# Kernel tuning notes

Measured on AMD Instinct MI355X. Metric: run time of the kernel, lower is better.

## Reference

```python
import jax, jax.numpy as jnp
import numpy as np
import math

B, S, D, H = 256, 200, 256, 8
DH = D // H
EPS = 1e-6
GELU_C = math.sqrt(2.0 / math.pi)


def layer_norm(x, a, b):
    # torch LayerNorm variant: unbiased std, eps added to std (not var)
    mean = jnp.mean(x, axis=-1, keepdims=True)
    std = jnp.sqrt(jnp.var(x, axis=-1, keepdims=True, ddof=1))
    return a * (x - mean) / (std + EPS) + b


def setup_inputs() -> dict:
    key = jax.random.key(0)
    ks = jax.random.split(key, 12)
    s = 0.02
    return {
        "hidden_img": jax.random.normal(ks[0], (B, S, D), jnp.float32),
        "hidden_title": jax.random.normal(ks[1], (B, S, D), jnp.float32),
        "mask": jax.random.randint(ks[2], (B, S), 0, 2, jnp.int32),
        "a_img": jnp.ones((D,), jnp.float32),
        "b_img": jnp.zeros((D,), jnp.float32),
        "a_title": jnp.ones((D,), jnp.float32),
        "b_title": jnp.zeros((D,), jnp.float32),
        "Wb": jax.random.normal(ks[3], (D, D), jnp.float32) * s,
        "bb": jnp.zeros((D,), jnp.float32),
        "Wo": jax.random.normal(ks[4], (D, D), jnp.float32) * s,
        "bo": jnp.zeros((D,), jnp.float32),
        "scale_attn": jax.random.normal(ks[5], (H, S), jnp.float32) * 0.5 + 1.0,
        "a_out": jnp.ones((D,), jnp.float32),
        "b_out": jnp.zeros((D,), jnp.float32),
        "W1": jax.random.normal(ks[6], (D, D), jnp.float32) * s,
        "b1": jnp.zeros((D,), jnp.float32),
        "scale_ffn": jax.random.normal(ks[7], (S, 1), jnp.float32) * 0.5 + 1.0,
    }


def reference(hidden_img, hidden_title, mask, a_img, b_img, a_title, b_title,
              Wb, bb, Wo, bo, scale_attn, a_out, b_out, W1, b1, scale_ffn):
    img_n = layer_norm(hidden_img, a_img, b_img)      # q = k = v
    title_n = layer_norm(hidden_title, a_title, b_title)

    # heads
    qkv = img_n.reshape(B, S, H, DH)                   # bshd
    k_b = (title_n @ Wb.T + bb).reshape(B, S, H, DH)

    # scores: q.k + q.k_b, scaled, per-head/per-query learned scale
    corr = jnp.einsum("bqhd,bkhd->bhqk", qkv, qkv)
    corr = corr + jnp.einsum("bqhd,bkhd->bhqk", qkv, k_b)
    corr = corr / math.sqrt(DH)
    corr = corr * scale_attn[None, :, :, None]         # [1,H,S,1]

    # key mask [B,S] -> [B,1,1,S]
    corr = jnp.where(mask[:, None, None, :] == 0, -1e9, corr)
    prob = jax.nn.softmax(corr, axis=-1)

    ctx = jnp.einsum("bhqk,bkhd->bqhd", prob, qkv).reshape(B, S, D)
    attn_out = ctx @ Wo.T + bo

    # residual 1 (dropout is identity in eval)
    h1 = hidden_img + attn_out

    # pre-norm FFN with learned positional scale + tanh-GELU
    h1_n = layer_norm(h1, a_out, b_out)
    z = scale_ffn[None] * (h1_n @ W1.T + b1)           # [B,S,D]
    act = 0.5 * z * (1.0 + jnp.tanh(GELU_C * (z + 0.044715 * z ** 3)))

    return h1 + act
```

## Files before the change

kernel.cpp:

```cpp
#include <hip/hip_runtime.h>
#include <math.h>

#define B_ 256
#define S_ 200
#define D_ 256
#define H_ 8
#define DH_ 32
#define BS_ (B_*S_)
#define NEL ((size_t)BS_*D_)

typedef __attribute__((ext_vector_type(8))) short bhalf8;
typedef __attribute__((ext_vector_type(4))) float fx4;

__device__ __forceinline__ unsigned short f2bf(float f) {
  union { float f; unsigned u; } x; x.f = f;
  unsigned r = x.u + 0x7FFFu + ((x.u >> 16) & 1u);
  return (unsigned short)(r >> 16);
}

__device__ __forceinline__ bhalf8 pack8(float4 a, float4 b) {
  bhalf8 p;
  p[0] = (short)f2bf(a.x); p[1] = (short)f2bf(a.y);
  p[2] = (short)f2bf(a.z); p[3] = (short)f2bf(a.w);
  p[4] = (short)f2bf(b.x); p[5] = (short)f2bf(b.y);
  p[6] = (short)f2bf(b.z); p[7] = (short)f2bf(b.w);
  return p;
}

__device__ __forceinline__ float wave_reduce_sum(float v) {
#pragma unroll
  for (int o = 32; o >= 1; o >>= 1) v += __shfl_xor(v, o, 64);
  return v;
}

__global__ __launch_bounds__(256) void ln_kernel(
    const float* __restrict__ x, const float* __restrict__ a,
    const float* __restrict__ b, float* __restrict__ y, int nrows) {
  int wave = threadIdx.x >> 6, lane = threadIdx.x & 63;
  int row = blockIdx.x * 4 + wave;
  if (row >= nrows) return;
  float4 v = ((const float4*)(x + (size_t)row * D_))[lane];
  float s  = v.x + v.y + v.z + v.w;
  float ss = v.x*v.x + v.y*v.y + v.z*v.z + v.w*v.w;
  s = wave_reduce_sum(s); ss = wave_reduce_sum(ss);
  float mean = s * (1.0f / D_);
  float var  = fmaxf((ss - (float)D_ * mean * mean) * (1.0f / (D_ - 1)), 0.0f);
  float inv  = 1.0f / (sqrtf(var) + 1e-6f);
  float4 av = ((const float4*)a)[lane];
  float4 bv = ((const float4*)b)[lane];
  float4 o;
  o.x = av.x * (v.x - mean) * inv + bv.x;
  o.y = av.y * (v.y - mean) * inv + bv.y;
  o.z = av.z * (v.z - mean) * inv + bv.z;
  o.w = av.w * (v.w - mean) * inv + bv.w;
  ((float4*)(y + (size_t)row * D_))[lane] = o;
}

__global__ __launch_bounds__(256) void rowstats_kernel(
    const float* __restrict__ x, float2* __restrict__ st, int nrows) {
  int wave = threadIdx.x >> 6, lane = threadIdx.x & 63;
  int row = blockIdx.x * 4 + wave;
  if (row >= nrows) return;
  float4 v = ((const float4*)(x + (size_t)row * D_))[lane];
  float s  = v.x + v.y + v.z + v.w;
  float ss = v.x*v.x + v.y*v.y + v.z*v.z + v.w*v.w;
  s = wave_reduce_sum(s); ss = wave_reduce_sum(ss);
  if (lane == 0) {
    float mean = s * (1.0f / D_);
    float var  = fmaxf((ss - (float)D_ * mean * mean) * (1.0f / (D_ - 1)), 0.0f);
    st[row] = make_float2(mean, 1.0f / (sqrtf(var) + 1e-6f));
  }
}

template <int EPI>
__global__ __launch_bounds__(256) void gemm_mfma_kernel(
    const float* __restrict__ A, const float* __restrict__ W,
    const float* __restrict__ bias, const float* __restrict__ add,
    const float* __restrict__ sf, const float2* __restrict__ stats,
    const float* __restrict__ ga, const float* __restrict__ gb,
    float* __restrict__ out) {
  __shared__ short As[128 * 40];
  __shared__ short Ws[128 * 40];
  const int tid = threadIdx.x;
  const int n0 = blockIdx.x * 128, m0 = blockIdx.y * 128;
  const int wv = tid >> 6, lane = tid & 63, g = lane >> 4, cc = lane & 15;
  fx4 acc[2][8];
#pragma unroll
  for (int i = 0; i < 2; i++)
#pragma unroll
    for (int j = 0; j < 8; j++) acc[i][j] = (fx4){0.f, 0.f, 0.f, 0.f};

  for (int k0 = 0; k0 < D_; k0 += 32) {
#pragma unroll
    for (int s = 0; s < 2; s++) {
      const int i = tid + s * 256;
      const int row = i >> 2, c8 = (i & 3) * 8;
      const float* gp = A + (size_t)(m0 + row) * D_ + k0 + c8;
      float4 f0 = *(const float4*)gp, f1 = *(const float4*)(gp + 4);
      if (EPI == 1) {
        float2 stt = stats[m0 + row];
        float4 a0 = *(const float4*)(ga + k0 + c8), a1 = *(const float4*)(ga + k0 + c8 + 4);
        float4 b0 = *(const float4*)(gb + k0 + c8), b1 = *(const float4*)(gb + k0 + c8 + 4);
        f0.x = (f0.x - stt.x) * stt.y * a0.x + b0.x;
        f0.y = (f0.y - stt.x) * stt.y * a0.y + b0.y;
        f0.z = (f0.z - stt.x) * stt.y * a0.z + b0.z;
        f0.w = (f0.w - stt.x) * stt.y * a0.w + b0.w;
        f1.x = (f1.x - stt.x) * stt.y * a1.x + b1.x;
        f1.y = (f1.y - stt.x) * stt.y * a1.y + b1.y;
        f1.z = (f1.z - stt.x) * stt.y * a1.z + b1.z;
        f1.w = (f1.w - stt.x) * stt.y * a1.w + b1.w;
      }
      *(bhalf8*)&As[row * 40 + c8] = pack8(f0, f1);
      const float* wp = W + (size_t)(n0 + row) * D_ + k0 + c8;
      float4 w0 = *(const float4*)wp, w1 = *(const float4*)(wp + 4);
      *(bhalf8*)&Ws[row * 40 + c8] = pack8(w0, w1);
    }
    __syncthreads();
    bhalf8 fa0 = *(const bhalf8*)&As[(wv * 32 + cc) * 40 + g * 8];
    bhalf8 fa1 = *(const bhalf8*)&As[(wv * 32 + 16 + cc) * 40 + g * 8];
#pragma unroll
    for (int j = 0; j < 8; j++) {
      bhalf8 fb = *(const bhalf8*)&Ws[(j * 16 + cc) * 40 + g * 8];
      acc[0][j] = __builtin_amdgcn_mfma_f32_16x16x32_bf16(fa0, fb, acc[0][j], 0, 0, 0);
      acc[1][j] = __builtin_amdgcn_mfma_f32_16x16x32_bf16(fa1, fb, acc[1][j], 0, 0, 0);
    }
    __syncthreads();
  }

#pragma unroll
  for (int i = 0; i < 2; i++)
#pragma unroll
    for (int j = 0; j < 8; j++)
#pragma unroll
      for (int r = 0; r < 4; r++) {
        const int m = m0 + wv * 32 + i * 16 + 4 * g + r;
        const int n = n0 + j * 16 + cc;
        float cv = acc[i][j][r] + bias[n];
        if (EPI == 0) {
          cv += add[(size_t)m * D_ + n];
        } else {
          const int srow = m % S_;
          float z = cv * sf[srow];
          float t3 = z + 0.044715f * z * z * z;
          float gl = 0.5f * z * (1.0f + tanhf(0.79788456080286536f * t3));
          cv = add[(size_t)m * D_ + n] + gl;
        }
        out[(size_t)m * D_ + n] = cv;
      }
}

__global__ __launch_bounds__(256) void attn_mfma_kernel(
    const float* __restrict__ img_n, const float* __restrict__ kk,
    const int* __restrict__ mask, const float* __restrict__ scale_attn,
    float* __restrict__ ctx) {
  __shared__ short K_s[208 * 40];
  __shared__ short Vt_s[32 * 216];
  __shared__ short P_s[4][16 * 224];
  __shared__ int   m_s[224];
  const int tid = threadIdx.x;
  const int b = blockIdx.x >> 3, h = blockIdx.x & 7;
  const size_t base = (size_t)b * (S_ * D_) + h * DH_;

  for (int i = tid; i < 800; i += 256) {
    const int row = i >> 2, c8 = (i & 3) * 8;
    const float* gp = kk + base + (size_t)row * D_ + c8;
    float4 f0 = *(const float4*)gp, f1 = *(const float4*)(gp + 4);
    *(bhalf8*)&K_s[row * 40 + c8] = pack8(f0, f1);
  }
  for (int i = tid; i < 1600; i += 256) {
    const int row = i >> 3, d4 = (i & 7) * 4;
    const float4 f = *(const float4*)(img_n + base + (size_t)row * D_ + d4);
    Vt_s[(d4 + 0) * 216 + row] = (short)f2bf(f.x);
    Vt_s[(d4 + 1) * 216 + row] = (short)f2bf(f.y);
    Vt_s[(d4 + 2) * 216 + row] = (short)f2bf(f.z);
    Vt_s[(d4 + 3) * 216 + row] = (short)f2bf(f.w);
  }
  { const int row = 200 + (tid >> 5), col = tid & 31; K_s[row * 40 + col] = 0; }
  for (int i = tid; i < 512; i += 256) { const int d = i >> 4, k = 200 + (i & 15); Vt_s[d * 216 + k] = 0; }
  if (tid < 224) m_s[tid] = (tid < S_) ? mask[b * S_ + tid] : 0;

  const int wv = tid >> 6, lane = tid & 63;
  const int g = lane >> 4, c = lane & 15;
  char* Pw = (char*)&P_s[wv][0];
  {
    const int row = lane >> 2, cb = 208 + (lane & 3) * 4;
#pragma unroll
    for (int j = 0; j < 4; j++) {
      const int col = cb + j;
      *(short*)(Pw + row * 448 + ((col * 2) ^ ((row >> 2) << 4))) = 0;
    }
  }
  __syncthreads();

  const float rs32 = 0.17677669529663687f;
  const fx4 zero = {0.f, 0.f, 0.f, 0.f};
  for (int t = wv; t < 13; t += 4) {
    const int q0 = t * 16;
    int qr = q0 + c; if (qr > S_ - 1) qr = S_ - 1;
    const float* qp = img_n + base + (size_t)qr * D_ + g * 8;
    bhalf8 af = pack8(*(const float4*)qp, *(const float4*)(qp + 4));

    fx4 st[13];
#pragma unroll
    for (int t2 = 0; t2 < 13; t2++) {
      bhalf8 kf = *(const bhalf8*)&K_s[(t2 * 16 + c) * 40 + g * 8];
      st[t2] = __builtin_amdgcn_mfma_f32_16x16x32_bf16(af, kf, zero, 0, 0, 0);
    }
    float sc[4], mx[4], l[4];
#pragma unroll
    for (int r = 0; r < 4; r++) {
      int q = q0 + 4 * g + r; if (q > S_ - 1) q = S_ - 1;
      sc[r] = scale_attn[h * S_ + q] * rs32;
      mx[r] = -1e30f; l[r] = 0.f;
    }
#pragma unroll
    for (int t2 = 0; t2 < 13; t2++) {
      const int msk = m_s[t2 * 16 + c];
#pragma unroll
      for (int r = 0; r < 4; r++) {
        float s = (msk != 0) ? st[t2][r] * sc[r] : -1e30f;
        st[t2][r] = s;
        mx[r] = fmaxf(mx[r], s);
      }
    }
#pragma unroll
    for (int r = 0; r < 4; r++) {
      mx[r] = fmaxf(mx[r], __shfl_xor(mx[r], 1));
      mx[r] = fmaxf(mx[r], __shfl_xor(mx[r], 2));
      mx[r] = fmaxf(mx[r], __shfl_xor(mx[r], 4));
      mx[r] = fmaxf(mx[r], __shfl_xor(mx[r], 8));
    }
#pragma unroll
    for (int t2 = 0; t2 < 13; t2++) {
#pragma unroll
      for (int r = 0; r < 4; r++) {
        float p = __expf(st[t2][r] - mx[r]);
        l[r] += p;
        const int row = 4 * g + r;
        *(short*)(Pw + row * 448 + (((t2 * 16 + c) * 2) ^ ((row >> 2) << 4))) = (short)f2bf(p);
      }
    }
#pragma unroll
    for (int r = 0; r < 4; r++) {
      l[r] += __shfl_xor(l[r], 1);
      l[r] += __shfl_xor(l[r], 2);
      l[r] += __shfl_xor(l[r], 4);
      l[r] += __shfl_xor(l[r], 8);
    }
    fx4 o0 = zero, o1 = zero;
#pragma unroll
    for (int ch = 0; ch < 7; ch++) {
      bhalf8 pf = *(const bhalf8*)(Pw + c * 448 + (((ch * 32 + g * 8) * 2) ^ ((c >> 2) << 4)));
      bhalf8 v0 = *(const bhalf8*)&Vt_s[c * 216 + ch * 32 + g * 8];
      bhalf8 v1 = *(const bhalf8*)&Vt_s[(16 + c) * 216 + ch * 32 + g * 8];
      o0 = __builtin_amdgcn_mfma_f32_16x16x32_bf16(pf, v0, o0, 0, 0, 0);
      o1 = __builtin_amdgcn_mfma_f32_16x16x32_bf16(pf, v1, o1, 0, 0, 0);
    }
#pragma unroll
    for (int r = 0; r < 4; r++) {
      const int q = q0 + 4 * g + r;
      if (q < S_) {
        const float inv = 1.0f / l[r];
        ctx[base + (size_t)q * D_ + c]      = o0[r] * inv;
        ctx[base + (size_t)q * D_ + 16 + c] = o1[r] * inv;
      }
    }
  }
}

extern "C" void kernel_launch(void* const* d_in, const int* in_sizes, int n_in,
                              void* d_out, int out_size, void* d_ws, size_t ws_size,
                              hipStream_t stream) {
  const float* hidden_img   = (const float*)d_in[0];
  const float* hidden_title = (const float*)d_in[1];
  const int*   mask         = (const int*)d_in[2];
  const float* a_img   = (const float*)d_in[3];
  const float* b_img   = (const float*)d_in[4];
  const float* a_title = (const float*)d_in[5];
  const float* b_title = (const float*)d_in[6];
  const float* Wb = (const float*)d_in[7];
  const float* bb = (const float*)d_in[8];
  const float* Wo = (const float*)d_in[9];
  const float* bo = (const float*)d_in[10];
  const float* scale_attn = (const float*)d_in[11];
  const float* a_out = (const float*)d_in[12];
  const float* b_out = (const float*)d_in[13];
  const float* W1 = (const float*)d_in[14];
  const float* b1 = (const float*)d_in[15];
  const float* scale_ffn = (const float*)d_in[16];
  float* out = (float*)d_out;

  float* ws    = (float*)d_ws;
  float* img_n = ws;
  float* kkbuf = ws + NEL;
  float* tbuf  = ws + 2 * NEL;
  float2* stats = (float2*)(ws + 3 * NEL);

  ln_kernel<<<dim3(BS_ / 4), 256, 0, stream>>>(hidden_img,   a_img,   b_img,   img_n, BS_);
  ln_kernel<<<dim3(BS_ / 4), 256, 0, stream>>>(hidden_title, a_title, b_title, tbuf,  BS_);
  gemm_mfma_kernel<0><<<dim3(2, 400), 256, 0, stream>>>(tbuf, Wb, bb, img_n,
                                                        nullptr, nullptr, nullptr, nullptr, kkbuf);
  attn_mfma_kernel<<<dim3(B_ * H_), 256, 0, stream>>>(img_n, kkbuf, mask, scale_attn, tbuf);
  gemm_mfma_kernel<0><<<dim3(2, 400), 256, 0, stream>>>(tbuf, Wo, bo, hidden_img,
                                                        nullptr, nullptr, nullptr, nullptr, kkbuf);
  rowstats_kernel<<<dim3(BS_ / 4), 256, 0, stream>>>(kkbuf, stats, BS_);
  gemm_mfma_kernel<1><<<dim3(2, 400), 256, 0, stream>>>(kkbuf, W1, b1, kkbuf,
                                                        scale_ffn, stats, a_out, b_out, out);
}
```

Measured before the change: 404.3 us.

## Store intermediates in bf16, fuse LayerNorms into GEMM epilogues, restructure GEMM tiling

Intermediates (normalized inputs, keys, context, post-residual LayerNorm) are now stored as bf16 instead of fp32, which roughly halves the HBM traffic between kernels. The weights are converted to bf16 once, and each GEMM block keeps the full 256x256 weight tile in LDS. Each wave covers 32 rows by the full N width, with register prefetch of A. The two input LayerNorms are merged into one launch, and the output LayerNorm statistics are computed inside the Wo GEMM epilogue, removing the separate rowstats pass. The attention kernel reads bf16 directly, uses padded LDS in place of XOR swizzles, and adds setprio around its MFMA sections. The residual added to the keys is now the bf16-rounded copy, which adds some precision risk.

```diff
diff --git a/kernel.cpp b/kernel.cpp
--- a/kernel.cpp
+++ b/kernel.cpp
@@ -17,7 +17,9 @@
   unsigned r = x.u + 0x7FFFu + ((x.u >> 16) & 1u);
   return (unsigned short)(r >> 16);
 }
-
+__device__ __forceinline__ float bf2f(unsigned short h) {
+  union { unsigned u; float f; } x; x.u = ((unsigned)h) << 16; return x.f;
+}
 __device__ __forceinline__ bhalf8 pack8(float4 a, float4 b) {
   bhalf8 p;
   p[0] = (short)f2bf(a.x); p[1] = (short)f2bf(a.y);
@@ -26,19 +28,34 @@
   p[6] = (short)f2bf(b.z); p[7] = (short)f2bf(b.w);
   return p;
 }
-
 __device__ __forceinline__ float wave_reduce_sum(float v) {
 #pragma unroll
   for (int o = 32; o >= 1; o >>= 1) v += __shfl_xor(v, o, 64);
   return v;
 }
 
-__global__ __launch_bounds__(256) void ln_kernel(
-    const float* __restrict__ x, const float* __restrict__ a,
-    const float* __restrict__ b, float* __restrict__ y, int nrows) {
-  int wave = threadIdx.x >> 6, lane = threadIdx.x & 63;
-  int row = blockIdx.x * 4 + wave;
-  if (row >= nrows) return;
+__global__ __launch_bounds__(256) void conv_w_kernel(
+    const float* __restrict__ Wb, const float* __restrict__ Wo,
+    const float* __restrict__ W1, short* __restrict__ dst) {
+  const int t = blockIdx.x * 256 + threadIdx.x;
+  const int w = t >> 13, r = (t & 8191) * 8;
+  const float* src = (w == 0) ? Wb : ((w == 1) ? Wo : W1);
+  float4 f0 = *(const float4*)(src + r), f1 = *(const float4*)(src + r + 4);
+  *(bhalf8*)(dst + (w << 16) + r) = pack8(f0, f1);
+}
+
+__global__ __launch_bounds__(256) void ln2_kernel(
+    const float* __restrict__ ximg, const float* __restrict__ xtit,
+    const float* __restrict__ a_img, const float* __restrict__ b_img,
+    const float* __restrict__ a_tit, const float* __restrict__ b_tit,
+    short* __restrict__ yimg, short* __restrict__ ytit) {
+  const int wave = threadIdx.x >> 6, lane = threadIdx.x & 63;
+  const int second = (blockIdx.x >= BS_ / 4) ? 1 : 0;
+  const int row = (blockIdx.x - second * (BS_ / 4)) * 4 + wave;
+  const float* x = second ? xtit : ximg;
+  const float* a = second ? a_tit : a_img;
+  const float* b = second ? b_tit : b_img;
+  short* y = second ? ytit : yimg;
   float4 v = ((const float4*)(x + (size_t)row * D_))[lane];
   float s  = v.x + v.y + v.z + v.w;
   float ss = v.x*v.x + v.y*v.y + v.z*v.z + v.w*v.w;
@@ -48,148 +65,158 @@
   float inv  = 1.0f / (sqrtf(var) + 1e-6f);
   float4 av = ((const float4*)a)[lane];
   float4 bv = ((const float4*)b)[lane];
-  float4 o;
-  o.x = av.x * (v.x - mean) * inv + bv.x;
-  o.y = av.y * (v.y - mean) * inv + bv.y;
-  o.z = av.z * (v.z - mean) * inv + bv.z;
-  o.w = av.w * (v.w - mean) * inv + bv.w;
-  ((float4*)(y + (size_t)row * D_))[lane] = o;
-}
-
-__global__ __launch_bounds__(256) void rowstats_kernel(
-    const float* __restrict__ x, float2* __restrict__ st, int nrows) {
-  int wave = threadIdx.x >> 6, lane = threadIdx.x & 63;
-  int row = blockIdx.x * 4 + wave;
-  if (row >= nrows) return;
-  float4 v = ((const float4*)(x + (size_t)row * D_))[lane];
-  float s  = v.x + v.y + v.z + v.w;
-  float ss = v.x*v.x + v.y*v.y + v.z*v.z + v.w*v.w;
-  s = wave_reduce_sum(s); ss = wave_reduce_sum(ss);
-  if (lane == 0) {
-    float mean = s * (1.0f / D_);
-    float var  = fmaxf((ss - (float)D_ * mean * mean) * (1.0f / (D_ - 1)), 0.0f);
-    st[row] = make_float2(mean, 1.0f / (sqrtf(var) + 1e-6f));
-  }
+  ushort4 o;
+  o.x = f2bf(av.x * (v.x - mean) * inv + bv.x);
+  o.y = f2bf(av.y * (v.y - mean) * inv + bv.y);
+  o.z = f2bf(av.z * (v.z - mean) * inv + bv.z);
+  o.w = f2bf(av.w * (v.w - mean) * inv + bv.w);
+  *(ushort4*)(y + (size_t)row * D_ + lane * 4) = o;
 }
 
 template <int EPI>
-__global__ __launch_bounds__(256) void gemm_mfma_kernel(
-    const float* __restrict__ A, const float* __restrict__ W,
-    const float* __restrict__ bias, const float* __restrict__ add,
-    const float* __restrict__ sf, const float2* __restrict__ stats,
+__global__ __launch_bounds__(512, 2) void gemm_k(
+    const short* __restrict__ A, const short* __restrict__ W,
+    const float* __restrict__ bias,
+    const short* __restrict__ addb,
+    const float* __restrict__ addf,
     const float* __restrict__ ga, const float* __restrict__ gb,
-    float* __restrict__ out) {
-  __shared__ short As[128 * 40];
-  __shared__ short Ws[128 * 40];
+    const float* __restrict__ sf,
+    short* __restrict__ outb, float* __restrict__ outf) {
+  __shared__ short Ws[256 * 260];
   const int tid = threadIdx.x;
-  const int n0 = blockIdx.x * 128, m0 = blockIdx.y * 128;
+  for (int cid = tid; cid < 8192; cid += 512) {
+    const int row = cid >> 5, ch = cid & 31;
+    *(bhalf8*)&Ws[row * 260 + ch * 8] = *(const bhalf8*)(W + row * 256 + ch * 8);
+  }
+  __syncthreads();
+
   const int wv = tid >> 6, lane = tid & 63, g = lane >> 4, cc = lane & 15;
-  fx4 acc[2][8];
+  const int mrow0 = blockIdx.x * 256 + wv * 32;
+  fx4 acc[2][16];
 #pragma unroll
   for (int i = 0; i < 2; i++)
 #pragma unroll
-    for (int j = 0; j < 8; j++) acc[i][j] = (fx4){0.f, 0.f, 0.f, 0.f};
-
-  for (int k0 = 0; k0 < D_; k0 += 32) {
-#pragma unroll
-    for (int s = 0; s < 2; s++) {
-      const int i = tid + s * 256;
-      const int row = i >> 2, c8 = (i & 3) * 8;
-      const float* gp = A + (size_t)(m0 + row) * D_ + k0 + c8;
-      float4 f0 = *(const float4*)gp, f1 = *(const float4*)(gp + 4);
-      if (EPI == 1) {
-        float2 stt = stats[m0 + row];
-        float4 a0 = *(const float4*)(ga + k0 + c8), a1 = *(const float4*)(ga + k0 + c8 + 4);
-        float4 b0 = *(const float4*)(gb + k0 + c8), b1 = *(const float4*)(gb + k0 + c8 + 4);
-        f0.x = (f0.x - stt.x) * stt.y * a0.x + b0.x;
-        f0.y = (f0.y - stt.x) * stt.y * a0.y + b0.y;
-        f0.z = (f0.z - stt.x) * stt.y * a0.z + b0.z;
-        f0.w = (f0.w - stt.x) * stt.y * a0.w + b0.w;
-        f1.x = (f1.x - stt.x) * stt.y * a1.x + b1.x;
-        f1.y = (f1.y - stt.x) * stt.y * a1.y + b1.y;
-        f1.z = (f1.z - stt.x) * stt.y * a1.z + b1.z;
-        f1.w = (f1.w - stt.x) * stt.y * a1.w + b1.w;
-      }
-      *(bhalf8*)&As[row * 40 + c8] = pack8(f0, f1);
-      const float* wp = W + (size_t)(n0 + row) * D_ + k0 + c8;
-      float4 w0 = *(const float4*)wp, w1 = *(const float4*)(wp + 4);
-      *(bhalf8*)&Ws[row * 40 + c8] = pack8(w0, w1);
-    }
-    __syncthreads();
-    bhalf8 fa0 = *(const bhalf8*)&As[(wv * 32 + cc) * 40 + g * 8];
-    bhalf8 fa1 = *(const bhalf8*)&As[(wv * 32 + 16 + cc) * 40 + g * 8];
-#pragma unroll
-    for (int j = 0; j < 8; j++) {
-      bhalf8 fb = *(const bhalf8*)&Ws[(j * 16 + cc) * 40 + g * 8];
-      acc[0][j] = __builtin_amdgcn_mfma_f32_16x16x32_bf16(fa0, fb, acc[0][j], 0, 0, 0);
-      acc[1][j] = __builtin_amdgcn_mfma_f32_16x16x32_bf16(fa1, fb, acc[1][j], 0, 0, 0);
-    }
-    __syncthreads();
-  }
-
-#pragma unroll
-  for (int i = 0; i < 2; i++)
-#pragma unroll
-    for (int j = 0; j < 8; j++)
-#pragma unroll
-      for (int r = 0; r < 4; r++) {
-        const int m = m0 + wv * 32 + i * 16 + 4 * g + r;
-        const int n = n0 + j * 16 + cc;
-        float cv = acc[i][j][r] + bias[n];
-        if (EPI == 0) {
-          cv += add[(size_t)m * D_ + n];
-        } else {
-          const int srow = m % S_;
-          float z = cv * sf[srow];
-          float t3 = z + 0.044715f * z * z * z;
-          float gl = 0.5f * z * (1.0f + tanhf(0.79788456080286536f * t3));
-          cv = add[(size_t)m * D_ + n] + gl;
+    for (int j = 0; j < 16; j++) acc[i][j] = (fx4){0.f, 0.f, 0.f, 0.f};
+
+  bhalf8 a0 = *(const bhalf8*)(A + (size_t)(mrow0 + cc) * D_ + g * 8);
+  bhalf8 a1 = *(const bhalf8*)(A + (size_t)(mrow0 + 16 + cc) * D_ + g * 8);
+#pragma unroll
+  for (int kc = 0; kc < 8; kc++) {
+    bhalf8 n0, n1;
+    if (kc < 7) {
+      n0 = *(const bhalf8*)(A + (size_t)(mrow0 + cc) * D_ + (kc + 1) * 32 + g * 8);
+      n1 = *(const bhalf8*)(A + (size_t)(mrow0 + 16 + cc) * D_ + (kc + 1) * 32 + g * 8);
+    }
+#pragma unroll
+    for (int j = 0; j < 16; j++) {
+      bhalf8 fb = *(const bhalf8*)&Ws[(j * 16 + cc) * 260 + kc * 32 + g * 8];
+      acc[0][j] = __builtin_amdgcn_mfma_f32_16x16x32_bf16(a0, fb, acc[0][j], 0, 0, 0);
+      acc[1][j] = __builtin_amdgcn_mfma_f32_16x16x32_bf16(a1, fb, acc[1][j], 0, 0, 0);
+    }
+    a0 = n0; a1 = n1;
+  }
+
+  float bias_r[16];
+#pragma unroll
+  for (int j = 0; j < 16; j++) bias_r[j] = bias[j * 16 + cc];
+
+  if (EPI == 0) {
+#pragma unroll
+    for (int i = 0; i < 2; i++)
+#pragma unroll
+      for (int r = 0; r < 4; r++) {
+        const size_t m = mrow0 + i * 16 + 4 * g + r;
+#pragma unroll
+        for (int j = 0; j < 16; j++) {
+          const int n = j * 16 + cc;
+          float v = acc[i][j][r] + bias_r[j] + bf2f((unsigned short)addb[m * D_ + n]);
+          outb[m * D_ + n] = (short)f2bf(v);
         }
-        out[(size_t)m * D_ + n] = cv;
-      }
+      }
+  } else if (EPI == 1) {
+    float ga_r[16], gb_r[16];
+#pragma unroll
+    for (int j = 0; j < 16; j++) { ga_r[j] = ga[j * 16 + cc]; gb_r[j] = gb[j * 16 + cc]; }
+#pragma unroll
+    for (int i = 0; i < 2; i++)
+#pragma unroll
+      for (int r = 0; r < 4; r++) {
+        const size_t m = mrow0 + i * 16 + 4 * g + r;
+        float s = 0.f, ss = 0.f;
+#pragma unroll
+        for (int j = 0; j < 16; j++) {
+          const int n = j * 16 + cc;
+          float v = acc[i][j][r] + bias_r[j] + addf[m * D_ + n];
+          outf[m * D_ + n] = v;
+          acc[i][j][r] = v;
+          s += v; ss += v * v;
+        }
+        s  += __shfl_xor(s, 1);  s += __shfl_xor(s, 2);  s += __shfl_xor(s, 4);  s += __shfl_xor(s, 8);
+        ss += __shfl_xor(ss, 1); ss += __shfl_xor(ss, 2); ss += __shfl_xor(ss, 4); ss += __shfl_xor(ss, 8);
+        const float mean = s * (1.0f / D_);
+        const float var  = fmaxf((ss * (1.0f / D_) - mean * mean) * ((float)D_ / (D_ - 1)), 0.0f);
+        const float inv  = 1.0f / (sqrtf(var) + 1e-6f);
+#pragma unroll
+        for (int j = 0; j < 16; j++) {
+          const int n = j * 16 + cc;
+          float h = (acc[i][j][r] - mean) * inv * ga_r[j] + gb_r[j];
+          outb[m * D_ + n] = (short)f2bf(h);
+        }
+      }
+  } else {
+#pragma unroll
+    for (int i = 0; i < 2; i++)
+#pragma unroll
+      for (int r = 0; r < 4; r++) {
+        const size_t m = mrow0 + i * 16 + 4 * g + r;
+        const float sfr = sf[(int)(m % S_)];
+#pragma unroll
+        for (int j = 0; j < 16; j++) {
+          const int n = j * 16 + cc;
+          float z = (acc[i][j][r] + bias_r[j]) * sfr;
+          float gl = 0.5f * z * (1.0f + tanhf(0.79788456080286536f * (z + 0.044715f * z * z * z)));
+          outf[m * D_ + n] = addf[m * D_ + n] + gl;
+        }
+      }
+  }
 }
 
 __global__ __launch_bounds__(256) void attn_mfma_kernel(
-    const float* __restrict__ img_n, const float* __restrict__ kk,
+    const short* __restrict__ imgb, const short* __restrict__ kkb,
     const int* __restrict__ mask, const float* __restrict__ scale_attn,
-    float* __restrict__ ctx) {
+    short* __restrict__ ctxb) {
   __shared__ short K_s[208 * 40];
-  __shared__ short Vt_s[32 * 216];
-  __shared__ short P_s[4][16 * 224];
+  __shared__ short Vt_s[32 * 232];
+  __shared__ short P_s[4][16 * 232];
   __shared__ int   m_s[224];
   const int tid = threadIdx.x;
   const int b = blockIdx.x >> 3, h = blockIdx.x & 7;
-  const size_t base = (size_t)b * (S_ * D_) + h * DH_;
+  const size_t base2 = (size_t)(b * S_) * D_ + h * DH_;
 
   for (int i = tid; i < 800; i += 256) {
-    const int row = i >> 2, c8 = (i & 3) * 8;
-    const float* gp = kk + base + (size_t)row * D_ + c8;
-    float4 f0 = *(const float4*)gp, f1 = *(const float4*)(gp + 4);
-    *(bhalf8*)&K_s[row * 40 + c8] = pack8(f0, f1);
-  }
-  for (int i = tid; i < 1600; i += 256) {
-    const int row = i >> 3, d4 = (i & 7) * 4;
-    const float4 f = *(const float4*)(img_n + base + (size_t)row * D_ + d4);
-    Vt_s[(d4 + 0) * 216 + row] = (short)f2bf(f.x);
-    Vt_s[(d4 + 1) * 216 + row] = (short)f2bf(f.y);
-    Vt_s[(d4 + 2) * 216 + row] = (short)f2bf(f.z);
-    Vt_s[(d4 + 3) * 216 + row] = (short)f2bf(f.w);
+    const int row = i >> 2, ch = i & 3;
+    *(bhalf8*)&K_s[row * 40 + ch * 8] = *(const bhalf8*)(kkb + base2 + (size_t)row * D_ + ch * 8);
+  }
+  for (int t = tid; t < 400; t += 256) {
+    const int p = t >> 2, ch = t & 3;
+    bhalf8 lo = *(const bhalf8*)(imgb + base2 + (size_t)(2 * p) * D_ + ch * 8);
+    bhalf8 hi = *(const bhalf8*)(imgb + base2 + (size_t)(2 * p + 1) * D_ + ch * 8);
+#pragma unroll
+    for (int u = 0; u < 8; u++) {
+      unsigned dw = (unsigned)(unsigned short)lo[u] | ((unsigned)(unsigned short)hi[u] << 16);
+      *(unsigned*)&Vt_s[(ch * 8 + u) * 232 + 2 * p] = dw;
+    }
   }
   { const int row = 200 + (tid >> 5), col = tid & 31; K_s[row * 40 + col] = 0; }
-  for (int i = tid; i < 512; i += 256) { const int d = i >> 4, k = 200 + (i & 15); Vt_s[d * 216 + k] = 0; }
+  { const int row = tid >> 3, k0 = 200 + (tid & 7) * 4;
+    *(unsigned long long*)&Vt_s[row * 232 + k0] = 0ULL; }
   if (tid < 224) m_s[tid] = (tid < S_) ? mask[b * S_ + tid] : 0;
 
   const int wv = tid >> 6, lane = tid & 63;
   const int g = lane >> 4, c = lane & 15;
-  char* Pw = (char*)&P_s[wv][0];
-  {
-    const int row = lane >> 2, cb = 208 + (lane & 3) * 4;
-#pragma unroll
-    for (int j = 0; j < 4; j++) {
-      const int col = cb + j;
-      *(short*)(Pw + row * 448 + ((col * 2) ^ ((row >> 2) << 4))) = 0;
-    }
-  }
+  short* Pw = &P_s[wv][0];
+  { const int row = lane >> 2, colq = lane & 3;
+    *(unsigned long long*)&Pw[row * 232 + 208 + colq * 4] = 0ULL; }
   __syncthreads();
 
   const float rs32 = 0.17677669529663687f;
@@ -197,15 +224,16 @@
   for (int t = wv; t < 13; t += 4) {
     const int q0 = t * 16;
     int qr = q0 + c; if (qr > S_ - 1) qr = S_ - 1;
-    const float* qp = img_n + base + (size_t)qr * D_ + g * 8;
-    bhalf8 af = pack8(*(const float4*)qp, *(const float4*)(qp + 4));
+    bhalf8 af = *(const bhalf8*)(imgb + base2 + (size_t)qr * D_ + g * 8);
 
     fx4 st[13];
+    __builtin_amdgcn_s_setprio(1);
 #pragma unroll
     for (int t2 = 0; t2 < 13; t2++) {
       bhalf8 kf = *(const bhalf8*)&K_s[(t2 * 16 + c) * 40 + g * 8];
       st[t2] = __builtin_amdgcn_mfma_f32_16x16x32_bf16(af, kf, zero, 0, 0, 0);
     }
+    __builtin_amdgcn_s_setprio(0);
     float sc[4], mx[4], l[4];
 #pragma unroll
     for (int r = 0; r < 4; r++) {
@@ -236,8 +264,7 @@
       for (int r = 0; r < 4; r++) {
         float p = __expf(st[t2][r] - mx[r]);
         l[r] += p;
-        const int row = 4 * g + r;
-        *(short*)(Pw + row * 448 + (((t2 * 16 + c) * 2) ^ ((row >> 2) << 4))) = (short)f2bf(p);
+        Pw[(4 * g + r) * 232 + t2 * 16 + c] = (short)f2bf(p);
       }
     }
 #pragma unroll
@@ -248,21 +275,23 @@
       l[r] += __shfl_xor(l[r], 8);
     }
     fx4 o0 = zero, o1 = zero;
+    __builtin_amdgcn_s_setprio(1);
 #pragma unroll
     for (int ch = 0; ch < 7; ch++) {
-      bhalf8 pf = *(const bhalf8*)(Pw + c * 448 + (((ch * 32 + g * 8) * 2) ^ ((c >> 2) << 4)));
-      bhalf8 v0 = *(const bhalf8*)&Vt_s[c * 216 + ch * 32 + g * 8];
-      bhalf8 v1 = *(const bhalf8*)&Vt_s[(16 + c) * 216 + ch * 32 + g * 8];
+      bhalf8 pf = *(const bhalf8*)&Pw[c * 232 + ch * 32 + g * 8];
+      bhalf8 v0 = *(const bhalf8*)&Vt_s[c * 232 + ch * 32 + g * 8];
+      bhalf8 v1 = *(const bhalf8*)&Vt_s[(16 + c) * 232 + ch * 32 + g * 8];
       o0 = __builtin_amdgcn_mfma_f32_16x16x32_bf16(pf, v0, o0, 0, 0, 0);
       o1 = __builtin_amdgcn_mfma_f32_16x16x32_bf16(pf, v1, o1, 0, 0, 0);
     }
+    __builtin_amdgcn_s_setprio(0);
 #pragma unroll
     for (int r = 0; r < 4; r++) {
       const int q = q0 + 4 * g + r;
       if (q < S_) {
         const float inv = 1.0f / l[r];
-        ctx[base + (size_t)q * D_ + c]      = o0[r] * inv;
-        ctx[base + (size_t)q * D_ + 16 + c] = o1[r] * inv;
+        ctxb[base2 + (size_t)q * D_ + c]      = (short)f2bf(o0[r] * inv);
+        ctxb[base2 + (size_t)q * D_ + 16 + c] = (short)f2bf(o1[r] * inv);
       }
     }
   }
@@ -290,20 +319,22 @@
   const float* scale_ffn = (const float*)d_in[16];
   float* out = (float*)d_out;
 
-  float* ws    = (float*)d_ws;
-  float* img_n = ws;
-  float* kkbuf = ws + NEL;
-  float* tbuf  = ws + 2 * NEL;
-  float2* stats = (float2*)(ws + 3 * NEL);
-
-  ln_kernel<<<dim3(BS_ / 4), 256, 0, stream>>>(hidden_img,   a_img,   b_img,   img_n, BS_);
-  ln_kernel<<<dim3(BS_ / 4), 256, 0, stream>>>(hidden_title, a_title, b_title, tbuf,  BS_);
-  gemm_mfma_kernel<0><<<dim3(2, 400), 256, 0, stream>>>(tbuf, Wb, bb, img_n,
-                                                        nullptr, nullptr, nullptr, nullptr, kkbuf);
-  attn_mfma_kernel<<<dim3(B_ * H_), 256, 0, stream>>>(img_n, kkbuf, mask, scale_attn, tbuf);
-  gemm_mfma_kernel<0><<<dim3(2, 400), 256, 0, stream>>>(tbuf, Wo, bo, hidden_img,
-                                                        nullptr, nullptr, nullptr, nullptr, kkbuf);
-  rowstats_kernel<<<dim3(BS_ / 4), 256, 0, stream>>>(kkbuf, stats, BS_);
-  gemm_mfma_kernel<1><<<dim3(2, 400), 256, 0, stream>>>(kkbuf, W1, b1, kkbuf,
-                                                        scale_ffn, stats, a_out, b_out, out);
-}
+  char* wsb = (char*)d_ws;
+  short* img_nb = (short*)(wsb);
+  short* kkb    = (short*)(wsb + 26214400);
+  short* ctxb   = (short*)(wsb + 52428800);
+  float* h1     = (float*)(wsb + 78643200);
+  short* h1nb   = (short*)(wsb + 131072000);
+  short* w16    = (short*)(wsb + 157286400);
+
+  conv_w_kernel<<<dim3(96), 256, 0, stream>>>(Wb, Wo, W1, w16);
+  ln2_kernel<<<dim3(2 * BS_ / 4), 256, 0, stream>>>(hidden_img, hidden_title,
+      a_img, b_img, a_title, b_title, img_nb, ctxb);
+  gemm_k<0><<<dim3(200), 512, 0, stream>>>(ctxb, w16, bb, img_nb,
+      nullptr, nullptr, nullptr, nullptr, kkb, nullptr);
+  attn_mfma_kernel<<<dim3(B_ * H_), 256, 0, stream>>>(img_nb, kkb, mask, scale_attn, ctxb);
+  gemm_k<1><<<dim3(200), 512, 0, stream>>>(ctxb, w16 + 65536, bo, nullptr,
+      hidden_img, a_out, b_out, nullptr, h1nb, h1);
+  gemm_k<2><<<dim3(200), 512, 0, stream>>>(h1nb, w16 + 131072, b1, nullptr,
+      h1, nullptr, nullptr, scale_ffn, nullptr, out);
+}
```

Result: no change. 397.7 us (-1.6%).
